# Optimization experiments

Hardware: AMD Instinct MI355X
Metric: run time of the kernel (lower is better)

## Reference

```python
import jax, jax.numpy as jnp
import numpy as np

B, L, S, M, N = 128, 3, 256, 256, 20000
NS, A, NL = 4, 5, 2
MAP_RANGE = 10.0
DELTA_VAR = 0.1
EPS = 1e-5


def _ln(x):
    mu = jnp.mean(x, -1, keepdims=True)
    var = jnp.var(x, -1, keepdims=True)
    return (x - mu) / jnp.sqrt(var + EPS)


def _cal_map_last(map_pts, anchor_last):
    # map_pts: [2, N], anchor_last: [B, 1, L] -> [B, M, 2]
    pos = anchor_last[:, 0, 0:2]
    d = map_pts[None, :, :] - pos[:, :, None]                    # [B,2,N]
    th = anchor_last[:, 0, -1]
    c, s = jnp.cos(th), jnp.sin(th)
    rot = jnp.stack([jnp.stack([c, s], -1), jnp.stack([-s, c], -1)], 1)  # [B,2,2]
    m = jnp.einsum('bij,bjn->bin', rot, d)                       # ego-frame points
    dis = jnp.sqrt(jnp.sum(m * m, axis=1, keepdims=True))        # [B,1,N]
    m = jnp.where(dis >= MAP_RANGE, 1e10, m)
    m = jnp.sort(m, axis=-1)                                     # per-coordinate sort (as in torch)
    m = jnp.where(m >= 1e9, 0.0, m)
    m = m[:, :, :M]                                              # torch F.pad negative pad == crop to map_num_max
    return jnp.transpose(m, (0, 2, 1))


def _forward(inp_start_point, map_pts, end_point, delta_limit_mean,
             W_enc_anchor, Wq, Wk, Wv, W_in, W_out, W_map1, W_map2,
             W_ih0, W_ih1, W_hh0, W_hh1, W_m1, W_m2, W_v1, W_v2):
    anchor = inp_start_point
    var_last = jnp.ones_like(anchor) * 0.01  # never updated, as in torch source
    pre_mean, pre_var, views = [], [], []
    scale = 1.0 / np.sqrt(S)                 # MHA 1 head -> head_dim = S
    bsz = anchor.shape[0]
    for step in range(NS):
        dm, dv = [anchor], [var_last]
        vt = [jnp.transpose(_cal_map_last(map_pts, anchor), (0, 2, 1))]
        h = jnp.ones((NL, bsz, S), anchor.dtype)
        c = jnp.ones((NL, bsz, S), anchor.dtype)
        for _ in range(A - 1):
            enc_a = _ln(jnp.concatenate([anchor, anchor - end_point, var_last], -1) @ W_enc_anchor[step].T)  # [B,1,S]
            ml = jax.lax.stop_gradient(_cal_map_last(map_pts, anchor))  # torch.no_grad in encode_last_map
            q = ml @ Wq[step].T
            k = ml @ Wk[step].T
            v = ml @ Wv[step].T
            wq, wk, wv = jnp.split(W_in[step], 3, axis=0)
            q2 = q @ wq.T
            k2 = k @ wk.T
            v2 = v @ wv.T
            attn = jax.nn.softmax(jnp.einsum('bqs,bks->bqk', q2, k2) * scale, axis=-1)
            o = jnp.einsum('bqk,bks->bqs', attn, v2) @ W_out[step].T    # [B,M,S]
            x = jax.nn.relu(jnp.transpose(o, (0, 2, 1)))                # [B,S,M]
            x = jax.nn.relu(x @ W_map1[step].T) @ W_map2[step].T        # [B,S,1]
            enc_m = _ln(jnp.transpose(x, (0, 2, 1)))                    # [B,1,S]
            xl = jnp.concatenate([enc_a, enc_m], -1)[:, 0, :]           # [B,2S], single LSTM timestep
            hs, cs = [], []
            for l, (Wih, Whh) in enumerate(((W_ih0[step], W_hh0[step]), (W_ih1[step], W_hh1[step]))):
                g = xl @ Wih.T + h[l] @ Whh.T
                i_g, f_g, g_g, o_g = jnp.split(g, 4, -1)               # torch gate order i,f,g,o
                cl = jax.nn.sigmoid(f_g) * c[l] + jax.nn.sigmoid(i_g) * jnp.tanh(g_g)
                hl = jax.nn.sigmoid(o_g) * jnp.tanh(cl)
                hs.append(hl)
                cs.append(cl)
                xl = hl
            h, c = jnp.stack(hs), jnp.stack(cs)
            mn = _ln(xl)[:, None, :]                                    # [B,1,S]
            mean = jnp.tanh(jax.nn.relu(jax.nn.relu(mn) @ W_m1[step].T) @ W_m2[step].T) * delta_limit_mean + anchor
            varr = jax.nn.sigmoid(jax.nn.relu(jax.nn.relu(mn) @ W_v1[step].T) @ W_v2[step].T) * DELTA_VAR
            dm.append(mean)
            dv.append(varr)
            anchor = mean
            vt.append(jnp.transpose(_cal_map_last(map_pts, anchor), (0, 2, 1)))
        pre_mean.append(jnp.concatenate(dm, 1)[:, None])    # [B,1,A,L]
        pre_var.append(jnp.concatenate(dv, 1)[:, None])
        views.append(jnp.stack(vt, 1)[:, None])             # [B,1,A,2,M]
    return (jnp.concatenate(pre_mean, 1), jnp.concatenate(pre_var, 1), jnp.concatenate(views, 1))


def setup_inputs() -> dict:
    key = jax.random.key(0)
    ks = jax.random.split(key, 20)

    def w(k, shape, fan):
        return jax.random.normal(k, shape, jnp.float32) / np.sqrt(fan)

    return {
        'inp_start_point': jax.random.normal(ks[0], (B, 1, L), jnp.float32) * 2.0,
        'map_pts': jax.random.uniform(ks[1], (2, N), jnp.float32, -50.0, 50.0),
        'end_point': jnp.array([5.0, 5.0, 0.0], jnp.float32),
        'delta_limit_mean': jnp.array([1.0, 1.0, 0.3], jnp.float32),
        'W_enc_anchor': w(ks[2], (NS, S, 3 * L), 3 * L),
        'Wq': w(ks[3], (NS, S, 2), 2),
        'Wk': w(ks[4], (NS, S, 2), 2),
        'Wv': w(ks[5], (NS, S, 2), 2),
        'W_in': w(ks[6], (NS, 3 * S, S), S),
        'W_out': w(ks[7], (NS, S, S), S),
        'W_map1': w(ks[8], (NS, S, M), M),
        'W_map2': w(ks[9], (NS, 1, S), S),
        'W_ih0': w(ks[10], (NS, 4 * S, 2 * S), 2 * S),
        'W_ih1': w(ks[11], (NS, 4 * S, S), S),
        'W_hh0': w(ks[12], (NS, 4 * S, S), S),
        'W_hh1': w(ks[13], (NS, 4 * S, S), S),
        'W_m1': w(ks[14], (NS, S, S), S),
        'W_m2': w(ks[15], (NS, L, S), S),
        'W_v1': w(ks[16], (NS, S, S), S),
        'W_v2': w(ks[17], (NS, L, S), S),
    }


def reference(inp_start_point, map_pts, end_point, delta_limit_mean,
              W_enc_anchor, Wq, Wk, Wv, W_in, W_out, W_map1, W_map2,
              W_ih0, W_ih1, W_hh0, W_hh1, W_m1, W_m2, W_v1, W_v2):
    return _forward(inp_start_point, map_pts, end_point, delta_limit_mean,
                    W_enc_anchor, Wq, Wk, Wv, W_in, W_out, W_map1, W_map2,
                    W_ih0, W_ih1, W_hh0, W_hh1, W_m1, W_m2, W_v1, W_v2)
```

## Files before the change

### kernel.cpp

```cpp
#include <hip/hip_runtime.h>

#define BB 128
#define NPTS 20000
#define NSTEP 4
#define NITER 4
#define MT 1024

#define OFF_ANCHOR 0
#define OFF_G      384
#define OFF_AO     400
#define OFF_U      2448
#define OFF_XL     67984
#define OFF_H      166288
#define OFF_C      231824
#define OFF_GB     297360
#define OFF_RMN    428432
#define OFF_TM     461200
#define OFF_TV     493968

#define OUT_VAR   7680
#define OUT_VIEWS 15360

__device__ __forceinline__ float sigf(float x){ return 1.0f/(1.0f+expf(-x)); }

__device__ __forceinline__ float blockSum256(float v, float* buf){
    for (int off = 32; off > 0; off >>= 1) v += __shfl_down(v, off, 64);
    int tid = threadIdx.x;
    __syncthreads();
    if ((tid & 63) == 0) buf[tid >> 6] = v;
    __syncthreads();
    return (buf[0] + buf[1]) + (buf[2] + buf[3]);
}

__device__ __forceinline__ float blockSum256g(float v, float* buf, int tid){
    for (int off = 32; off > 0; off >>= 1) v += __shfl_down(v, off, 64);
    __syncthreads();
    if (tid < 256 && (tid & 63) == 0) buf[tid >> 6] = v;
    __syncthreads();
    return (buf[0] + buf[1]) + (buf[2] + buf[3]);
}

__device__ __forceinline__ double blockSum256d(double v, double* buf){
    for (int off = 32; off > 0; off >>= 1) v += __shfl_down(v, off, 64);
    int tid = threadIdx.x;
    __syncthreads();
    if ((tid & 63) == 0) buf[tid >> 6] = v;
    __syncthreads();
    return (buf[0] + buf[1]) + (buf[2] + buf[3]);
}

__global__ __launch_bounds__(256) void k_init(const float* __restrict__ inp, float* __restrict__ ws)
{
    int i = blockIdx.x*256 + threadIdx.x;
    if (i < BB*3) ws[OFF_ANCHOR + i] = inp[i];
}

__global__ __launch_bounds__(256) void k_pre(const float* __restrict__ Wq, const float* __restrict__ Wk,
                                             const float* __restrict__ Wv, const float* __restrict__ Win,
                                             const float* __restrict__ Wout, float* __restrict__ ws)
{
    __shared__ float wql[512], wkl[512], wvl[512];
    __shared__ double avl[512];
    __shared__ double dbuf[4];
    int s = blockIdx.x, t = threadIdx.x;
    wql[t] = Wq[s*512 + t];   wql[256+t] = Wq[s*512 + 256 + t];
    wkl[t] = Wk[s*512 + t];   wkl[256+t] = Wk[s*512 + 256 + t];
    wvl[t] = Wv[s*512 + t];   wvl[256+t] = Wv[s*512 + 256 + t];
    __syncthreads();
    const float* wq = Win + s*196608 + t*256;
    const float* wk = wq + 65536;
    const float* wv = wq + 131072;
    double aq0=0,aq1=0,ak0=0,ak1=0,av0=0,av1=0;
    for (int j = 0; j < 256; j++){
        double a = wq[j], b = wk[j], c = wv[j];
        aq0 += a*(double)wql[j*2]; aq1 += a*(double)wql[j*2+1];
        ak0 += b*(double)wkl[j*2]; ak1 += b*(double)wkl[j*2+1];
        av0 += c*(double)wvl[j*2]; av1 += c*(double)wvl[j*2+1];
    }
    avl[t*2] = av0; avl[t*2+1] = av1;
    double g00 = blockSum256d(aq0*ak0, dbuf);
    double g01 = blockSum256d(aq0*ak1, dbuf);
    double g10 = blockSum256d(aq1*ak0, dbuf);
    double g11 = blockSum256d(aq1*ak1, dbuf);
    if (t == 0){
        ws[OFF_G + s*4+0] = (float)g00; ws[OFF_G + s*4+1] = (float)g01;
        ws[OFF_G + s*4+2] = (float)g10; ws[OFF_G + s*4+3] = (float)g11;
    }
    const float* wo = Wout + s*65536 + t*256;
    double o0 = 0.0, o1 = 0.0;
    for (int j = 0; j < 256; j++){
        double w = wo[j];
        o0 += w*avl[j*2]; o1 += w*avl[j*2+1];
    }
    ws[OFF_AO + s*512 + t*2]   = (float)o0;
    ws[OFF_AO + s*512 + t*2+1] = (float)o1;
}

__global__ __launch_bounds__(MT) void k_mapenc(const float* __restrict__ mp, float* __restrict__ ws,
                                               float* __restrict__ out, const float* __restrict__ Wenc,
                                               const float* __restrict__ endp, int s, int t, int wprev)
{
    __shared__ unsigned int histx[256], histy[256];
    __shared__ float vx[1024], vy[1024];
    __shared__ float candx[448], candy[448];
    __shared__ float mxS[256], myS[256];
    __shared__ int scanx[256], scany[256];
    __shared__ int shjx, shjy;
    __shared__ unsigned int cnt_in, cntx, cnty;
    __shared__ float rbuf[4];
    int tid = threadIdx.x, b = blockIdx.x;
    float ax = ws[OFF_ANCHOR + b*3 + 0];
    float ay = ws[OFF_ANCHOR + b*3 + 1];
    float th = ws[OFF_ANCHOR + b*3 + 2];
    float cth = cosf(th), sth = sinf(th);
    if (tid < 256){ histx[tid] = 0u; histy[tid] = 0u; }
    if (tid == 0){ cnt_in = 0u; cntx = 0u; cnty = 0u; }
    __syncthreads();
    for (int i = tid; i < NPTS; i += MT){
        float dx = mp[i] - ax, dy = mp[NPTS + i] - ay;
        float rx = cth*dx + sth*dy;
        float ry = cth*dy - sth*dx;
        float d  = sqrtf(rx*rx + ry*ry);
        if (d < 10.0f){
            unsigned p = atomicAdd(&cnt_in, 1u);
            if (p < 1024u){ vx[p] = rx; vy[p] = ry; }
            int bx = min(max((int)((rx + 10.0f)*12.8f), 0), 255);
            int by = min(max((int)((ry + 10.0f)*12.8f), 0), 255);
            atomicAdd(&histx[bx], 1u); atomicAdd(&histy[by], 1u);
        }
    }
    __syncthreads();
    int total = (int)min(cnt_in, 1024u);
    int K = min(256, total);
    int px = 0, py = 0;
    if (tid < 256){
        px = (int)histx[tid]; py = (int)histy[tid];
        scanx[tid] = px; scany[tid] = py;
    }
    __syncthreads();
    for (int off = 1; off < 256; off <<= 1){
        int vxs = 0, vys = 0;
        if (tid < 256){
            vxs = (tid >= off) ? scanx[tid - off] : 0;
            vys = (tid >= off) ? scany[tid - off] : 0;
        }
        __syncthreads();
        if (tid < 256){ scanx[tid] += vxs; scany[tid] += vys; }
        __syncthreads();
    }
    if (K > 0){
        if (tid < 256){
            if (scanx[tid] - px < K && scanx[tid] >= K) shjx = tid;
            if (scany[tid] - py < K && scany[tid] >= K) shjy = tid;
        }
    } else if (tid == 0){ shjx = -1; shjy = -1; }
    __syncthreads();
    int jx = shjx, jy = shjy;
    for (int i = tid; i < total; i += MT){
        float v = vx[i];
        int bx = min(max((int)((v + 10.0f)*12.8f), 0), 255);
        if (bx <= jx){ unsigned p = atomicAdd(&cntx, 1u); if (p < 448u) candx[p] = v; }
        v = vy[i];
        int by = min(max((int)((v + 10.0f)*12.8f), 0), 255);
        if (by <= jy){ unsigned p = atomicAdd(&cnty, 1u); if (p < 448u) candy[p] = v; }
    }
    __syncthreads();
    int cx = (int)min(cntx, 448u), cy = (int)min(cnty, 448u);
    for (int i = tid; i < cx; i += MT){
        float v = candx[i];
        int r = 0;
        for (int j2 = 0; j2 < cx; j2++){
            float w2 = candx[j2];
            r += (w2 < v) || (w2 == v && j2 < i);
        }
        if (r < 256) mxS[r] = v;
    }
    for (int i = tid; i < cy; i += MT){
        float v = candy[i];
        int r = 0;
        for (int j2 = 0; j2 < cy; j2++){
            float w2 = candy[j2];
            r += (w2 < v) || (w2 == v && j2 < i);
        }
        if (r < 256) myS[r] = v;
    }
    __syncthreads();
    float mlx = 0.f, mly = 0.f;
    if (tid < 256){
        mlx = (tid < K) ? mxS[tid] : 0.0f;
        mly = (tid < K) ? myS[tid] : 0.0f;
        int obase = OUT_VIEWS + (((b*NSTEP + s)*5 + t)*2)*256;
        out[obase + tid]       = mlx;
        out[obase + 256 + tid] = mly;
        if (wprev){
            int pbase = OUT_VIEWS + (((b*NSTEP + (s-1))*5 + 4)*2)*256;
            out[pbase + tid]       = mlx;
            out[pbase + 256 + tid] = mly;
        }
    }
    if (t == 4) return;
    __syncthreads();
    if (tid < 256){ mxS[tid] = mlx; myS[tid] = mly; }
    __syncthreads();
    float accv = 0.f, dd = 0.f;
    if (tid < 256){
        float a0 = ax, a1 = ay, a2 = th;
        float z9[9] = {a0, a1, a2, a0-endp[0], a1-endp[1], a2-endp[2], 0.01f, 0.01f, 0.01f};
        const float* w = Wenc + s*2304 + tid*9;
        #pragma unroll
        for (int j2 = 0; j2 < 9; j2++) accv += z9[j2]*w[j2];
    }
    float mu = blockSum256g(accv, rbuf, tid) * (1.0f/256.0f);
    dd = accv - mu;
    float var = blockSum256g(tid < 256 ? dd*dd : 0.f, rbuf, tid) * (1.0f/256.0f);
    if (tid < 256)
        ws[OFF_XL + b*512 + tid] = dd * rsqrtf(var + 1e-5f);
    if (tid < 256){
        float g00 = ws[OFF_G + s*4+0], g01 = ws[OFF_G + s*4+1];
        float g10 = ws[OFF_G + s*4+2], g11 = ws[OFF_G + s*4+3];
        float xq = mxS[tid], yq = myS[tid];
        float t0 = g00*xq + g10*yq;
        float t1 = g01*xq + g11*yq;
        float mxv = -1e30f;
        for (int j2 = 0; j2 < 256; j2++){
            float l = (t0*mxS[j2] + t1*myS[j2]) * 0.0625f;
            mxv = fmaxf(mxv, l);
        }
        float sum = 0.f, ux = 0.f, uy = 0.f;
        for (int j2 = 0; j2 < 256; j2++){
            float l = (t0*mxS[j2] + t1*myS[j2]) * 0.0625f;
            float e = expf(l - mxv);
            sum += e; ux += e*mxS[j2]; uy += e*myS[j2];
        }
        float inv = 1.0f/sum;
        ws[OFF_U + b*512 + tid*2]   = ux*inv;
        ws[OFF_U + b*512 + tid*2+1] = uy*inv;
        if (t == 0){
            ws[OFF_H + b*256 + tid] = 1.0f;
            ws[OFF_H + BB*256 + b*256 + tid] = 1.0f;
            ws[OFF_C + b*256 + tid] = 1.0f;
            ws[OFF_C + BB*256 + b*256 + tid] = 1.0f;
            if (tid < 3){
                out[((b*NSTEP + s)*5 + 0)*3 + tid] = ws[OFF_ANCHOR + b*3 + tid];
                out[OUT_VAR + ((b*NSTEP + s)*5 + 0)*3 + tid] = 0.01f;
            }
        }
    }
}

__global__ __launch_bounds__(256) void k_big(float* __restrict__ ws, const float* __restrict__ W1,
                                             const float* __restrict__ W2, int s)
{
    __shared__ __align__(16) float ul[512];
    __shared__ float aol[128];
    __shared__ float w2l[64];
    __shared__ __align__(16) float xt[64*36];
    __shared__ __align__(16) float w1t[64*36];
    __shared__ float red[64*17];
    int sct = blockIdx.x, st = blockIdx.y, b = blockIdx.z;
    int tid = threadIdx.x, tx = tid & 15, ty = tid >> 4;
    {
        float2 uv = *(const float2*)(ws + OFF_U + b*512 + tid*2);
        ul[tid*2] = uv.x; ul[tid*2+1] = uv.y;
        if (tid < 128) aol[tid] = ws[OFF_AO + s*512 + st*128 + tid];
        if (tid < 64)  w2l[tid] = W2[sct*64 + tid];
    }
    __syncthreads();
    float acc[4][4];
    #pragma unroll
    for (int i=0;i<4;i++){
        #pragma unroll
        for (int j=0;j<4;j++) acc[i][j] = 0.f;
    }
    for (int mt = 0; mt < 8; mt++){
        {
            int cl = tid >> 2, f0 = tid & 3;
            const float* g = W1 + (sct*64 + cl)*256 + mt*32 + f0*4;
            float4 v0 = *(const float4*)g;
            float4 v1 = *(const float4*)(g + 16);
            *(float4*)(w1t + cl*36 + f0*4)      = v0;
            *(float4*)(w1t + cl*36 + f0*4 + 16) = v1;
        }
        {
            int r = tid >> 2, mg = tid & 3;
            float A0 = aol[r*2], A1 = aol[r*2+1];
            int m0 = mt*32 + mg*4;
            float4 o0, o1;
            o0.x = fmaxf(A0*ul[(m0+0)*2] + A1*ul[(m0+0)*2+1], 0.f);
            o0.y = fmaxf(A0*ul[(m0+1)*2] + A1*ul[(m0+1)*2+1], 0.f);
            o0.z = fmaxf(A0*ul[(m0+2)*2] + A1*ul[(m0+2)*2+1], 0.f);
            o0.w = fmaxf(A0*ul[(m0+3)*2] + A1*ul[(m0+3)*2+1], 0.f);
            int m1 = mt*32 + (mg+4)*4;
            o1.x = fmaxf(A0*ul[(m1+0)*2] + A1*ul[(m1+0)*2+1], 0.f);
            o1.y = fmaxf(A0*ul[(m1+1)*2] + A1*ul[(m1+1)*2+1], 0.f);
            o1.z = fmaxf(A0*ul[(m1+2)*2] + A1*ul[(m1+2)*2+1], 0.f);
            o1.w = fmaxf(A0*ul[(m1+3)*2] + A1*ul[(m1+3)*2+1], 0.f);
            *(float4*)(xt + r*36 + mg*4)     = o0;
            *(float4*)(xt + r*36 + (mg+4)*4) = o1;
        }
        __syncthreads();
        #pragma unroll
        for (int m4 = 0; m4 < 8; m4++){
            float4 xv[4], wv[4];
            #pragma unroll
            for (int i=0;i<4;i++) xv[i] = *(const float4*)(xt + (ty + 16*i)*36 + m4*4);
            #pragma unroll
            for (int j=0;j<4;j++) wv[j] = *(const float4*)(w1t + (tx + 16*j)*36 + m4*4);
            #pragma unroll
            for (int i=0;i<4;i++){
                #pragma unroll
                for (int j=0;j<4;j++){
                    acc[i][j] += xv[i].x*wv[j].x + xv[i].y*wv[j].y + xv[i].z*wv[j].z + xv[i].w*wv[j].w;
                }
            }
        }
        __syncthreads();
    }
    #pragma unroll
    for (int i=0;i<4;i++){
        float p = 0.f;
        #pragma unroll
        for (int j=0;j<4;j++) p += fmaxf(acc[i][j], 0.f) * w2l[tx + 16*j];
        red[(ty + 16*i)*17 + tx] = p;
    }
    __syncthreads();
    if (tid < 64){
        float sm = 0.f;
        #pragma unroll
        for (int q=0;q<16;q++) sm += red[tid*17 + q];
        ws[OFF_GB + b*1024 + sct*256 + st*64 + tid] = sm;
    }
}

__global__ __launch_bounds__(256) void k_lnencm(float* __restrict__ ws)
{
    __shared__ float rbuf[4];
    int b = blockIdx.x, t = threadIdx.x;
    const float* p = ws + OFF_GB + b*1024;
    float v = p[t];
    v += p[256+t]; v += p[512+t]; v += p[768+t];
    float mu = blockSum256(v, rbuf) * (1.0f/256.0f);
    float d = v - mu;
    float var = blockSum256(d*d, rbuf) * (1.0f/256.0f);
    ws[OFF_XL + b*512 + 256 + t] = d * rsqrtf(var + 1e-5f);
}

template<int K>
__device__ __forceinline__ void gemm_pass(const float* __restrict__ A, const float* __restrict__ W,
                                          float* As, float* Wsh, float (&acc)[2][4],
                                          int bt, int ot, int tid)
{
    int tx = tid & 15, ty = tid >> 4;
    for (int kt = 0; kt < K/32; kt++){
        {
            int bb = tid >> 3, kk = (tid & 7) * 4;
            float4 v = *(const float4*)(A + (bt*32+bb)*K + kt*32 + kk);
            float* ap = As + bb*33 + kk;
            ap[0]=v.x; ap[1]=v.y; ap[2]=v.z; ap[3]=v.w;
        }
        {
            int oo = tid >> 2, kk = (tid & 3) * 8;
            const float* g = W + (ot*64+oo)*K + kt*32 + kk;
            float4 v0 = *(const float4*)g;
            float4 v1 = *(const float4*)(g + 4);
            float* wp = Wsh + oo*33 + kk;
            wp[0]=v0.x; wp[1]=v0.y; wp[2]=v0.z; wp[3]=v0.w;
            wp[4]=v1.x; wp[5]=v1.y; wp[6]=v1.z; wp[7]=v1.w;
        }
        __syncthreads();
        #pragma unroll
        for (int kk = 0; kk < 32; kk++){
            float a0 = As[(ty*2)*33 + kk], a1 = As[(ty*2+1)*33 + kk];
            float w0 = Wsh[(tx*4)*33+kk],   w1 = Wsh[(tx*4+1)*33+kk];
            float w2 = Wsh[(tx*4+2)*33+kk], w3 = Wsh[(tx*4+3)*33+kk];
            acc[0][0] += a0*w0; acc[0][1] += a0*w1; acc[0][2] += a0*w2; acc[0][3] += a0*w3;
            acc[1][0] += a1*w0; acc[1][1] += a1*w1; acc[1][2] += a1*w2; acc[1][3] += a1*w3;
        }
        __syncthreads();
    }
}

template<int K1, int K2, int RELU>
__global__ __launch_bounds__(256) void k_gemm(const float* __restrict__ A1, const float* __restrict__ W1,
                                              const float* __restrict__ A2, const float* __restrict__ W2,
                                              float* __restrict__ C, int Osz)
{
    __shared__ float As[32*33];
    __shared__ float Wsh[64*33];
    int tid = threadIdx.x, tx = tid & 15, ty = tid >> 4;
    int ot = blockIdx.x, bt = blockIdx.y;
    float acc[2][4];
    #pragma unroll
    for (int i=0;i<2;i++){
        #pragma unroll
        for (int j=0;j<4;j++) acc[i][j]=0.f;
    }
    gemm_pass<K1>(A1, W1, As, Wsh, acc, bt, ot, tid);
    if constexpr (K2 > 0){
        gemm_pass<K2>(A2, W2, As, Wsh, acc, bt, ot, tid);
    }
    #pragma unroll
    for (int i=0;i<2;i++){
        float4 v;
        v.x = acc[i][0]; v.y = acc[i][1]; v.z = acc[i][2]; v.w = acc[i][3];
        if (RELU){ v.x=fmaxf(v.x,0.f); v.y=fmaxf(v.y,0.f); v.z=fmaxf(v.z,0.f); v.w=fmaxf(v.w,0.f); }
        *(float4*)(C + (bt*32+ty*2+i)*Osz + ot*64 + tx*4) = v;
    }
}

__global__ __launch_bounds__(256) void k_heads2(const float* __restrict__ A, const float* __restrict__ Wm1,
                                                const float* __restrict__ Wv1, float* __restrict__ ws)
{
    __shared__ float As[32*33];
    __shared__ float Wsh[64*33];
    int tid = threadIdx.x, tx = tid & 15, ty = tid >> 4;
    int bx = blockIdx.x, bt = blockIdx.y;
    int ot = bx & 3;
    const float* W = (bx < 4) ? Wm1 : Wv1;
    float* C = ws + ((bx < 4) ? OFF_TM : OFF_TV);
    float acc[2][4];
    #pragma unroll
    for (int i=0;i<2;i++){
        #pragma unroll
        for (int j=0;j<4;j++) acc[i][j]=0.f;
    }
    gemm_pass<256>(A, W, As, Wsh, acc, bt, ot, tid);
    #pragma unroll
    for (int i=0;i<2;i++){
        float4 v;
        v.x = fmaxf(acc[i][0],0.f); v.y = fmaxf(acc[i][1],0.f);
        v.z = fmaxf(acc[i][2],0.f); v.w = fmaxf(acc[i][3],0.f);
        *(float4*)(C + (bt*32+ty*2+i)*256 + ot*64 + tx*4) = v;
    }
}

__global__ __launch_bounds__(256) void k_gates(float* __restrict__ ws, int l)
{
    int b = blockIdx.x, t = threadIdx.x;
    const float* g = ws + OFF_GB + b*1024;
    float ig = g[t], fg = g[256+t], gg = g[512+t], og = g[768+t];
    int idx = l*BB*256 + b*256 + t;
    float cold = ws[OFF_C + idx];
    float cl = sigf(fg)*cold + sigf(ig)*tanhf(gg);
    float hl = sigf(og)*tanhf(cl);
    ws[OFF_C + idx] = cl;
    ws[OFF_H + idx] = hl;
}

__global__ __launch_bounds__(256) void k_mn(float* __restrict__ ws)
{
    __shared__ float rbuf[4];
    int b = blockIdx.x, t = threadIdx.x;
    const float* g = ws + OFF_GB + b*1024;
    float ig = g[t], fg = g[256+t], gg = g[512+t], og = g[768+t];
    int idx = BB*256 + b*256 + t;
    float cold = ws[OFF_C + idx];
    float cl = sigf(fg)*cold + sigf(ig)*tanhf(gg);
    float hl = sigf(og)*tanhf(cl);
    ws[OFF_C + idx] = cl;
    ws[OFF_H + idx] = hl;
    float mu = blockSum256(hl, rbuf) * (1.0f/256.0f);
    float d = hl - mu;
    float var = blockSum256(d*d, rbuf) * (1.0f/256.0f);
    ws[OFF_RMN + b*256 + t] = fmaxf(d * rsqrtf(var + 1e-5f), 0.0f);
}

__global__ __launch_bounds__(256) void k_head(const float* __restrict__ Wm2, const float* __restrict__ Wv2,
                                              const float* __restrict__ dlm, float* __restrict__ ws,
                                              float* __restrict__ out, int s, int t)
{
    int b = blockIdx.x, tid = threadIdx.x;
    int w = tid >> 6, lane = tid & 63;
    #pragma unroll
    for (int p = 0; p < 2; p++){
        int oi = p*4 + w;
        if (oi < 6){
            int j = (oi < 3) ? oi : oi - 3;
            const float* tb = ws + ((oi < 3) ? OFF_TM : OFF_TV) + b*256;
            const float* wr = ((oi < 3) ? Wm2 : Wv2) + j*256;
            float pa = 0.f;
            #pragma unroll
            for (int q = 0; q < 4; q++) pa += tb[lane + 64*q] * wr[lane + 64*q];
            for (int off = 32; off > 0; off >>= 1) pa += __shfl_down(pa, off, 64);
            if (lane == 0){
                if (oi < 3){
                    float mv = tanhf(pa) * dlm[j] + ws[OFF_ANCHOR + b*3 + j];
                    out[((b*NSTEP + s)*5 + (t+1))*3 + j] = mv;
                    ws[OFF_ANCHOR + b*3 + j] = mv;
                } else {
                    out[OUT_VAR + ((b*NSTEP + s)*5 + (t+1))*3 + j] = sigf(pa)*0.1f;
                }
            }
        }
    }
}

extern "C" void kernel_launch(void* const* d_in, const int* in_sizes, int n_in,
                              void* d_out, int out_size, void* d_ws, size_t ws_size,
                              hipStream_t stream)
{
    (void)in_sizes; (void)n_in; (void)out_size; (void)ws_size;
    const float* inp  = (const float*)d_in[0];
    const float* mp   = (const float*)d_in[1];
    const float* endp = (const float*)d_in[2];
    const float* dlm  = (const float*)d_in[3];
    const float* Wenc = (const float*)d_in[4];
    const float* Wq   = (const float*)d_in[5];
    const float* Wk   = (const float*)d_in[6];
    const float* Wv   = (const float*)d_in[7];
    const float* Win  = (const float*)d_in[8];
    const float* Wout = (const float*)d_in[9];
    const float* Wmap1= (const float*)d_in[10];
    const float* Wmap2= (const float*)d_in[11];
    const float* Wih0 = (const float*)d_in[12];
    const float* Wih1 = (const float*)d_in[13];
    const float* Whh0 = (const float*)d_in[14];
    const float* Whh1 = (const float*)d_in[15];
    const float* Wm1  = (const float*)d_in[16];
    const float* Wm2  = (const float*)d_in[17];
    const float* Wv1  = (const float*)d_in[18];
    const float* Wv2  = (const float*)d_in[19];
    float* out = (float*)d_out;
    float* ws  = (float*)d_ws;

    k_init<<<2, 256, 0, stream>>>(inp, ws);
    k_pre<<<NSTEP, 256, 0, stream>>>(Wq, Wk, Wv, Win, Wout, ws);
    for (int s = 0; s < NSTEP; s++){
        for (int t = 0; t < NITER; t++){
            k_mapenc<<<BB, MT, 0, stream>>>(mp, ws, out, Wenc, endp, s, t,
                                            (t == 0 && s > 0) ? 1 : 0);
            k_big<<<dim3(4, 4, BB), 256, 0, stream>>>(ws, Wmap1 + s*65536, Wmap2 + s*256, s);
            k_lnencm<<<BB, 256, 0, stream>>>(ws);
            k_gemm<512,256,0><<<dim3(16,4), 256, 0, stream>>>(ws+OFF_XL, Wih0 + s*524288,
                                                              ws+OFF_H,  Whh0 + s*262144,
                                                              ws+OFF_GB, 1024);
            k_gates<<<BB, 256, 0, stream>>>(ws, 0);
            k_gemm<256,256,0><<<dim3(16,4), 256, 0, stream>>>(ws+OFF_H,          Wih1 + s*262144,
                                                              ws+OFF_H + BB*256, Whh1 + s*262144,
                                                              ws+OFF_GB, 1024);
            k_mn<<<BB, 256, 0, stream>>>(ws);
            k_heads2<<<dim3(8,4), 256, 0, stream>>>(ws+OFF_RMN, Wm1 + s*65536, Wv1 + s*65536, ws);
            k_head<<<BB, 256, 0, stream>>>(Wm2 + s*768, Wv2 + s*768, dlm, ws, out, s, t);
        }
    }
    k_mapenc<<<BB, MT, 0, stream>>>(mp, ws, out, Wenc, endp, 3, 4, 0);
}
```

Before: 3.742 ms.

## Fuse LSTM, gate and head tail kernels into one cooperative kernel with grid syncs

Replaces the seven small per-iteration tail kernels (layer norm, two LSTM GEMMs, gates, norm, head GEMMs, final head) with a single cooperative kernel of 64 blocks that uses grid-wide syncs between phases. The aim is to cut kernel launch overhead and inter-kernel gaps across the 16 iterations. In exchange, the elementwise phases now run on 64 blocks, each handling two batch rows, where they previously had 128. Each grid.sync also has its own cost.

```diff
diff --git a/kernel.cpp b/kernel.cpp
--- a/kernel.cpp
+++ b/kernel.cpp
@@ -1,4 +1,7 @@
 #include <hip/hip_runtime.h>
+#include <hip/hip_cooperative_groups.h>
+
+namespace cg = cooperative_groups;
 
 #define BB 128
 #define NPTS 20000
@@ -332,19 +335,6 @@
     }
 }
 
-__global__ __launch_bounds__(256) void k_lnencm(float* __restrict__ ws)
-{
-    __shared__ float rbuf[4];
-    int b = blockIdx.x, t = threadIdx.x;
-    const float* p = ws + OFF_GB + b*1024;
-    float v = p[t];
-    v += p[256+t]; v += p[512+t]; v += p[768+t];
-    float mu = blockSum256(v, rbuf) * (1.0f/256.0f);
-    float d = v - mu;
-    float var = blockSum256(d*d, rbuf) * (1.0f/256.0f);
-    ws[OFF_XL + b*512 + 256 + t] = d * rsqrtf(var + 1e-5f);
-}
-
 template<int K>
 __device__ __forceinline__ void gemm_pass(const float* __restrict__ A, const float* __restrict__ W,
                                           float* As, float* Wsh, float (&acc)[2][4],
@@ -380,115 +370,145 @@
     }
 }
 
-template<int K1, int K2, int RELU>
-__global__ __launch_bounds__(256) void k_gemm(const float* __restrict__ A1, const float* __restrict__ W1,
-                                              const float* __restrict__ A2, const float* __restrict__ W2,
-                                              float* __restrict__ C, int Osz)
-{
+__global__ __launch_bounds__(256) void k_tail(
+    const float* __restrict__ Wih0, const float* __restrict__ Whh0,
+    const float* __restrict__ Wih1, const float* __restrict__ Whh1,
+    const float* __restrict__ Wm1, const float* __restrict__ Wv1,
+    const float* __restrict__ Wm2, const float* __restrict__ Wv2,
+    const float* __restrict__ dlm, float* __restrict__ ws, float* __restrict__ out,
+    int s, int t)
+{
+    cg::grid_group grid = cg::this_grid();
     __shared__ float As[32*33];
     __shared__ float Wsh[64*33];
-    int tid = threadIdx.x, tx = tid & 15, ty = tid >> 4;
-    int ot = blockIdx.x, bt = blockIdx.y;
-    float acc[2][4];
-    #pragma unroll
-    for (int i=0;i<2;i++){
-        #pragma unroll
-        for (int j=0;j<4;j++) acc[i][j]=0.f;
-    }
-    gemm_pass<K1>(A1, W1, As, Wsh, acc, bt, ot, tid);
-    if constexpr (K2 > 0){
-        gemm_pass<K2>(A2, W2, As, Wsh, acc, bt, ot, tid);
-    }
-    #pragma unroll
-    for (int i=0;i<2;i++){
-        float4 v;
-        v.x = acc[i][0]; v.y = acc[i][1]; v.z = acc[i][2]; v.w = acc[i][3];
-        if (RELU){ v.x=fmaxf(v.x,0.f); v.y=fmaxf(v.y,0.f); v.z=fmaxf(v.z,0.f); v.w=fmaxf(v.w,0.f); }
-        *(float4*)(C + (bt*32+ty*2+i)*Osz + ot*64 + tx*4) = v;
-    }
-}
-
-__global__ __launch_bounds__(256) void k_heads2(const float* __restrict__ A, const float* __restrict__ Wm1,
-                                                const float* __restrict__ Wv1, float* __restrict__ ws)
-{
-    __shared__ float As[32*33];
-    __shared__ float Wsh[64*33];
-    int tid = threadIdx.x, tx = tid & 15, ty = tid >> 4;
-    int bx = blockIdx.x, bt = blockIdx.y;
-    int ot = bx & 3;
-    const float* W = (bx < 4) ? Wm1 : Wv1;
-    float* C = ws + ((bx < 4) ? OFF_TM : OFF_TV);
-    float acc[2][4];
-    #pragma unroll
-    for (int i=0;i<2;i++){
-        #pragma unroll
-        for (int j=0;j<4;j++) acc[i][j]=0.f;
-    }
-    gemm_pass<256>(A, W, As, Wsh, acc, bt, ot, tid);
-    #pragma unroll
-    for (int i=0;i<2;i++){
-        float4 v;
-        v.x = fmaxf(acc[i][0],0.f); v.y = fmaxf(acc[i][1],0.f);
-        v.z = fmaxf(acc[i][2],0.f); v.w = fmaxf(acc[i][3],0.f);
-        *(float4*)(C + (bt*32+ty*2+i)*256 + ot*64 + tx*4) = v;
-    }
-}
-
-__global__ __launch_bounds__(256) void k_gates(float* __restrict__ ws, int l)
-{
-    int b = blockIdx.x, t = threadIdx.x;
-    const float* g = ws + OFF_GB + b*1024;
-    float ig = g[t], fg = g[256+t], gg = g[512+t], og = g[768+t];
-    int idx = l*BB*256 + b*256 + t;
-    float cold = ws[OFF_C + idx];
-    float cl = sigf(fg)*cold + sigf(ig)*tanhf(gg);
-    float hl = sigf(og)*tanhf(cl);
-    ws[OFF_C + idx] = cl;
-    ws[OFF_H + idx] = hl;
-}
-
-__global__ __launch_bounds__(256) void k_mn(float* __restrict__ ws)
-{
     __shared__ float rbuf[4];
-    int b = blockIdx.x, t = threadIdx.x;
-    const float* g = ws + OFF_GB + b*1024;
-    float ig = g[t], fg = g[256+t], gg = g[512+t], og = g[768+t];
-    int idx = BB*256 + b*256 + t;
-    float cold = ws[OFF_C + idx];
-    float cl = sigf(fg)*cold + sigf(ig)*tanhf(gg);
-    float hl = sigf(og)*tanhf(cl);
-    ws[OFF_C + idx] = cl;
-    ws[OFF_H + idx] = hl;
-    float mu = blockSum256(hl, rbuf) * (1.0f/256.0f);
-    float d = hl - mu;
-    float var = blockSum256(d*d, rbuf) * (1.0f/256.0f);
-    ws[OFF_RMN + b*256 + t] = fmaxf(d * rsqrtf(var + 1e-5f), 0.0f);
-}
-
-__global__ __launch_bounds__(256) void k_head(const float* __restrict__ Wm2, const float* __restrict__ Wv2,
-                                              const float* __restrict__ dlm, float* __restrict__ ws,
-                                              float* __restrict__ out, int s, int t)
-{
-    int b = blockIdx.x, tid = threadIdx.x;
-    int w = tid >> 6, lane = tid & 63;
-    #pragma unroll
-    for (int p = 0; p < 2; p++){
-        int oi = p*4 + w;
-        if (oi < 6){
-            int j = (oi < 3) ? oi : oi - 3;
-            const float* tb = ws + ((oi < 3) ? OFF_TM : OFF_TV) + b*256;
-            const float* wr = ((oi < 3) ? Wm2 : Wv2) + j*256;
-            float pa = 0.f;
+    int g = blockIdx.x, tid = threadIdx.x;
+    int tx = tid & 15, ty = tid >> 4;
+
+    for (int bb = 0; bb < 2; bb++){
+        int b = g*2 + bb;
+        const float* p = ws + OFF_GB + b*1024;
+        float v = p[tid];
+        v += p[256+tid]; v += p[512+tid]; v += p[768+tid];
+        float mu = blockSum256(v, rbuf) * (1.0f/256.0f);
+        float d = v - mu;
+        float var = blockSum256(d*d, rbuf) * (1.0f/256.0f);
+        ws[OFF_XL + b*512 + 256 + tid] = d * rsqrtf(var + 1e-5f);
+    }
+    grid.sync();
+
+    {
+        int ot = g & 15, bt = g >> 4;
+        float acc[2][4];
+        #pragma unroll
+        for (int i=0;i<2;i++){
             #pragma unroll
-            for (int q = 0; q < 4; q++) pa += tb[lane + 64*q] * wr[lane + 64*q];
-            for (int off = 32; off > 0; off >>= 1) pa += __shfl_down(pa, off, 64);
-            if (lane == 0){
-                if (oi < 3){
-                    float mv = tanhf(pa) * dlm[j] + ws[OFF_ANCHOR + b*3 + j];
-                    out[((b*NSTEP + s)*5 + (t+1))*3 + j] = mv;
-                    ws[OFF_ANCHOR + b*3 + j] = mv;
-                } else {
-                    out[OUT_VAR + ((b*NSTEP + s)*5 + (t+1))*3 + j] = sigf(pa)*0.1f;
+            for (int j=0;j<4;j++) acc[i][j]=0.f;
+        }
+        gemm_pass<512>(ws + OFF_XL, Wih0, As, Wsh, acc, bt, ot, tid);
+        gemm_pass<256>(ws + OFF_H,  Whh0, As, Wsh, acc, bt, ot, tid);
+        #pragma unroll
+        for (int i=0;i<2;i++){
+            float4 v;
+            v.x = acc[i][0]; v.y = acc[i][1]; v.z = acc[i][2]; v.w = acc[i][3];
+            *(float4*)(ws + OFF_GB + (bt*32+ty*2+i)*1024 + ot*64 + tx*4) = v;
+        }
+    }
+    grid.sync();
+
+    for (int bb = 0; bb < 2; bb++){
+        int b = g*2 + bb;
+        const float* gg_ = ws + OFF_GB + b*1024;
+        float ig = gg_[tid], fg = gg_[256+tid], ggv = gg_[512+tid], og = gg_[768+tid];
+        int idx = b*256 + tid;
+        float cold = ws[OFF_C + idx];
+        float cl = sigf(fg)*cold + sigf(ig)*tanhf(ggv);
+        float hl = sigf(og)*tanhf(cl);
+        ws[OFF_C + idx] = cl;
+        ws[OFF_H + idx] = hl;
+    }
+    grid.sync();
+
+    {
+        int ot = g & 15, bt = g >> 4;
+        float acc[2][4];
+        #pragma unroll
+        for (int i=0;i<2;i++){
+            #pragma unroll
+            for (int j=0;j<4;j++) acc[i][j]=0.f;
+        }
+        gemm_pass<256>(ws + OFF_H,          Wih1, As, Wsh, acc, bt, ot, tid);
+        gemm_pass<256>(ws + OFF_H + BB*256, Whh1, As, Wsh, acc, bt, ot, tid);
+        #pragma unroll
+        for (int i=0;i<2;i++){
+            float4 v;
+            v.x = acc[i][0]; v.y = acc[i][1]; v.z = acc[i][2]; v.w = acc[i][3];
+            *(float4*)(ws + OFF_GB + (bt*32+ty*2+i)*1024 + ot*64 + tx*4) = v;
+        }
+    }
+    grid.sync();
+
+    for (int bb = 0; bb < 2; bb++){
+        int b = g*2 + bb;
+        const float* gg_ = ws + OFF_GB + b*1024;
+        float ig = gg_[tid], fg = gg_[256+tid], ggv = gg_[512+tid], og = gg_[768+tid];
+        int idx = BB*256 + b*256 + tid;
+        float cold = ws[OFF_C + idx];
+        float cl = sigf(fg)*cold + sigf(ig)*tanhf(ggv);
+        float hl = sigf(og)*tanhf(cl);
+        ws[OFF_C + idx] = cl;
+        ws[OFF_H + idx] = hl;
+        float mu = blockSum256(hl, rbuf) * (1.0f/256.0f);
+        float d = hl - mu;
+        float var = blockSum256(d*d, rbuf) * (1.0f/256.0f);
+        ws[OFF_RMN + b*256 + tid] = fmaxf(d * rsqrtf(var + 1e-5f), 0.0f);
+    }
+    grid.sync();
+
+    if (g < 32){
+        int bx = g & 7, bt = g >> 3;
+        int ot = bx & 3;
+        const float* W = (bx < 4) ? Wm1 : Wv1;
+        float* C = ws + ((bx < 4) ? OFF_TM : OFF_TV);
+        float acc[2][4];
+        #pragma unroll
+        for (int i=0;i<2;i++){
+            #pragma unroll
+            for (int j=0;j<4;j++) acc[i][j]=0.f;
+        }
+        gemm_pass<256>(ws + OFF_RMN, W, As, Wsh, acc, bt, ot, tid);
+        #pragma unroll
+        for (int i=0;i<2;i++){
+            float4 v;
+            v.x = fmaxf(acc[i][0],0.f); v.y = fmaxf(acc[i][1],0.f);
+            v.z = fmaxf(acc[i][2],0.f); v.w = fmaxf(acc[i][3],0.f);
+            *(float4*)(C + (bt*32+ty*2+i)*256 + ot*64 + tx*4) = v;
+        }
+    }
+    grid.sync();
+
+    for (int bb = 0; bb < 2; bb++){
+        int b = g*2 + bb;
+        int w = tid >> 6, lane = tid & 63;
+        #pragma unroll
+        for (int p = 0; p < 2; p++){
+            int oi = p*4 + w;
+            if (oi < 6){
+                int j = (oi < 3) ? oi : oi - 3;
+                const float* tb = ws + ((oi < 3) ? OFF_TM : OFF_TV) + b*256;
+                const float* wr = ((oi < 3) ? Wm2 : Wv2) + j*256;
+                float pa = 0.f;
+                #pragma unroll
+                for (int q = 0; q < 4; q++) pa += tb[lane + 64*q] * wr[lane + 64*q];
+                for (int off = 32; off > 0; off >>= 1) pa += __shfl_down(pa, off, 64);
+                if (lane == 0){
+                    if (oi < 3){
+                        float mv = tanhf(pa) * dlm[j] + ws[OFF_ANCHOR + b*3 + j];
+                        out[((b*NSTEP + s)*5 + (t+1))*3 + j] = mv;
+                        ws[OFF_ANCHOR + b*3 + j] = mv;
+                    } else {
+                        out[OUT_VAR + ((b*NSTEP + s)*5 + (t+1))*3 + j] = sigf(pa)*0.1f;
+                    }
                 }
             }
         }
@@ -530,17 +550,25 @@
             k_mapenc<<<BB, MT, 0, stream>>>(mp, ws, out, Wenc, endp, s, t,
                                             (t == 0 && s > 0) ? 1 : 0);
             k_big<<<dim3(4, 4, BB), 256, 0, stream>>>(ws, Wmap1 + s*65536, Wmap2 + s*256, s);
-            k_lnencm<<<BB, 256, 0, stream>>>(ws);
-            k_gemm<512,256,0><<<dim3(16,4), 256, 0, stream>>>(ws+OFF_XL, Wih0 + s*524288,
-                                                              ws+OFF_H,  Whh0 + s*262144,
-                                                              ws+OFF_GB, 1024);
-            k_gates<<<BB, 256, 0, stream>>>(ws, 0);
-            k_gemm<256,256,0><<<dim3(16,4), 256, 0, stream>>>(ws+OFF_H,          Wih1 + s*262144,
-                                                              ws+OFF_H + BB*256, Whh1 + s*262144,
-                                                              ws+OFF_GB, 1024);
-            k_mn<<<BB, 256, 0, stream>>>(ws);
-            k_heads2<<<dim3(8,4), 256, 0, stream>>>(ws+OFF_RMN, Wm1 + s*65536, Wv1 + s*65536, ws);
-            k_head<<<BB, 256, 0, stream>>>(Wm2 + s*768, Wv2 + s*768, dlm, ws, out, s, t);
+            {
+                const float* a_ih0 = Wih0 + s*524288;
+                const float* a_hh0 = Whh0 + s*262144;
+                const float* a_ih1 = Wih1 + s*262144;
+                const float* a_hh1 = Whh1 + s*262144;
+                const float* a_m1  = Wm1 + s*65536;
+                const float* a_v1  = Wv1 + s*65536;
+                const float* a_m2  = Wm2 + s*768;
+                const float* a_v2  = Wv2 + s*768;
+                const float* a_dlm = dlm;
+                float* a_ws = ws;
+                float* a_out = out;
+                int sv = s, tv = t;
+                void* args[13] = {(void*)&a_ih0, (void*)&a_hh0, (void*)&a_ih1, (void*)&a_hh1,
+                                  (void*)&a_m1, (void*)&a_v1, (void*)&a_m2, (void*)&a_v2,
+                                  (void*)&a_dlm, (void*)&a_ws, (void*)&a_out, (void*)&sv, (void*)&tv};
+                hipLaunchCooperativeKernel((const void*)k_tail, dim3(64), dim3(256),
+                                           args, 0, stream);
+            }
         }
     }
     k_mapenc<<<BB, MT, 0, stream>>>(mp, ws, out, Wenc, endp, 3, 4, 0);
```

New measurement: 4.883 ms. +30.5%, slower.

## Fuse LSTM gates into layer-1 GEMM and merge heads; aggregate atomics per wavefront

Applied to the files above, without the earlier changes.

The layer-0 gate nonlinearity is folded into the layer-1 GEMM kernel. Each block recomputes h0 for its 32 batch rows into shared memory, and the cell state is ping-ponged between two buffers so blocks with different output tiles do not race on it. The layer-1 gates, layernorm, both head GEMMs and the final projections are fused into one per-batch kernel. This cuts five launches per iteration to two. In the map encoder, per-thread shared atomics are replaced with ballot and popcount wavefront-aggregated atomics. The cost is that gate math is now computed redundantly 16 times, and the per-batch kernel streams the full Wm1/Wv1 matrices once per batch row instead of sharing tiles across rows.

```diff
diff --git a/kernel.cpp b/kernel.cpp
--- a/kernel.cpp
+++ b/kernel.cpp
@@ -14,9 +14,8 @@
 #define OFF_H      166288
 #define OFF_C      231824
 #define OFF_GB     297360
-#define OFF_RMN    428432
-#define OFF_TM     461200
-#define OFF_TV     493968
+#define OFF_C0B    428432
+#define OFF_GB2    461200
 
 #define OUT_VAR   7680
 #define OUT_VIEWS 15360
@@ -109,6 +108,7 @@
     __shared__ unsigned int cnt_in, cntx, cnty;
     __shared__ float rbuf[4];
     int tid = threadIdx.x, b = blockIdx.x;
+    int lane = tid & 63;
     float ax = ws[OFF_ANCHOR + b*3 + 0];
     float ay = ws[OFF_ANCHOR + b*3 + 1];
     float th = ws[OFF_ANCHOR + b*3 + 2];
@@ -121,8 +121,15 @@
         float rx = cth*dx + sth*dy;
         float ry = cth*dy - sth*dx;
         float d  = sqrtf(rx*rx + ry*ry);
-        if (d < 10.0f){
-            unsigned p = atomicAdd(&cnt_in, 1u);
+        bool keep = (d < 10.0f);
+        unsigned long long mask = __ballot(keep);
+        if (keep){
+            unsigned long long lower = mask & ((1ull << lane) - 1ull);
+            int leader = __ffsll((unsigned long long)mask) - 1;
+            unsigned base = 0;
+            if (lane == leader) base = atomicAdd(&cnt_in, (unsigned)__popcll(mask));
+            base = __shfl(base, leader, 64);
+            unsigned p = base + (unsigned)__popcll(lower);
             if (p < 1024u){ vx[p] = rx; vy[p] = ry; }
             int bx = min(max((int)((rx + 10.0f)*12.8f), 0), 255);
             int by = min(max((int)((ry + 10.0f)*12.8f), 0), 255);
@@ -157,12 +164,30 @@
     __syncthreads();
     int jx = shjx, jy = shjy;
     for (int i = tid; i < total; i += MT){
-        float v = vx[i];
-        int bx = min(max((int)((v + 10.0f)*12.8f), 0), 255);
-        if (bx <= jx){ unsigned p = atomicAdd(&cntx, 1u); if (p < 448u) candx[p] = v; }
-        v = vy[i];
-        int by = min(max((int)((v + 10.0f)*12.8f), 0), 255);
-        if (by <= jy){ unsigned p = atomicAdd(&cnty, 1u); if (p < 448u) candy[p] = v; }
+        float vxa = vx[i], vya = vy[i];
+        int bx = min(max((int)((vxa + 10.0f)*12.8f), 0), 255);
+        int by = min(max((int)((vya + 10.0f)*12.8f), 0), 255);
+        bool kx = (bx <= jx), ky = (by <= jy);
+        unsigned long long mx_ = __ballot(kx);
+        if (kx){
+            unsigned long long lower = mx_ & ((1ull << lane) - 1ull);
+            int leader = __ffsll((unsigned long long)mx_) - 1;
+            unsigned base = 0;
+            if (lane == leader) base = atomicAdd(&cntx, (unsigned)__popcll(mx_));
+            base = __shfl(base, leader, 64);
+            unsigned p = base + (unsigned)__popcll(lower);
+            if (p < 448u) candx[p] = vxa;
+        }
+        unsigned long long my_ = __ballot(ky);
+        if (ky){
+            unsigned long long lower = my_ & ((1ull << lane) - 1ull);
+            int leader = __ffsll((unsigned long long)my_) - 1;
+            unsigned base = 0;
+            if (lane == leader) base = atomicAdd(&cnty, (unsigned)__popcll(my_));
+            base = __shfl(base, leader, 64);
+            unsigned p = base + (unsigned)__popcll(lower);
+            if (p < 448u) candy[p] = vya;
+        }
     }
     __syncthreads();
     int cx = (int)min(cntx, 448u), cy = (int)min(cnty, 448u);
@@ -380,6 +405,18 @@
     }
 }
 
+template<int K>
+__device__ __forceinline__ void stage_w(const float* __restrict__ W, float* Wsh, int ot, int kt, int tid)
+{
+    int oo = tid >> 2, kk = (tid & 3) * 8;
+    const float* g = W + (ot*64+oo)*K + kt*32 + kk;
+    float4 v0 = *(const float4*)g;
+    float4 v1 = *(const float4*)(g + 4);
+    float* wp = Wsh + oo*33 + kk;
+    wp[0]=v0.x; wp[1]=v0.y; wp[2]=v0.z; wp[3]=v0.w;
+    wp[4]=v1.x; wp[5]=v1.y; wp[6]=v1.z; wp[7]=v1.w;
+}
+
 template<int K1, int K2, int RELU>
 __global__ __launch_bounds__(256) void k_gemm(const float* __restrict__ A1, const float* __restrict__ W1,
                                               const float* __restrict__ A2, const float* __restrict__ W2,
@@ -408,87 +445,130 @@
     }
 }
 
-__global__ __launch_bounds__(256) void k_heads2(const float* __restrict__ A, const float* __restrict__ Wm1,
-                                                const float* __restrict__ Wv1, float* __restrict__ ws)
-{
+__global__ __launch_bounds__(256) void k_g256(const float* __restrict__ Wih1, const float* __restrict__ Whh1,
+                                              float* __restrict__ ws, int t)
+{
+    __shared__ float h0t[32*257];
     __shared__ float As[32*33];
     __shared__ float Wsh[64*33];
     int tid = threadIdx.x, tx = tid & 15, ty = tid >> 4;
-    int bx = blockIdx.x, bt = blockIdx.y;
-    int ot = bx & 3;
-    const float* W = (bx < 4) ? Wm1 : Wv1;
-    float* C = ws + ((bx < 4) ? OFF_TM : OFF_TV);
+    int ot = blockIdx.x, bt = blockIdx.y;
+    int crd = (t & 1) ? OFF_C0B : OFF_C;
+    int cwr = (t & 1) ? OFF_C : OFF_C0B;
+    for (int bb = 0; bb < 32; bb++){
+        int b = bt*32 + bb;
+        const float* g = ws + OFF_GB + b*1024;
+        float ig = g[tid], fg = g[256+tid], gg = g[512+tid], og = g[768+tid];
+        float cold = ws[crd + b*256 + tid];
+        float cl = sigf(fg)*cold + sigf(ig)*tanhf(gg);
+        float hl = sigf(og)*tanhf(cl);
+        ws[cwr + b*256 + tid] = cl;
+        ws[OFF_H + b*256 + tid] = hl;
+        h0t[bb*257 + tid] = hl;
+    }
+    __syncthreads();
     float acc[2][4];
     #pragma unroll
     for (int i=0;i<2;i++){
         #pragma unroll
         for (int j=0;j<4;j++) acc[i][j]=0.f;
     }
-    gemm_pass<256>(A, W, As, Wsh, acc, bt, ot, tid);
+    for (int kt = 0; kt < 8; kt++){
+        stage_w<256>(Wih1, Wsh, ot, kt, tid);
+        __syncthreads();
+        #pragma unroll
+        for (int kk = 0; kk < 32; kk++){
+            float a0 = h0t[(ty*2)*257 + kt*32 + kk], a1 = h0t[(ty*2+1)*257 + kt*32 + kk];
+            float w0 = Wsh[(tx*4)*33+kk],   w1 = Wsh[(tx*4+1)*33+kk];
+            float w2 = Wsh[(tx*4+2)*33+kk], w3 = Wsh[(tx*4+3)*33+kk];
+            acc[0][0] += a0*w0; acc[0][1] += a0*w1; acc[0][2] += a0*w2; acc[0][3] += a0*w3;
+            acc[1][0] += a1*w0; acc[1][1] += a1*w1; acc[1][2] += a1*w2; acc[1][3] += a1*w3;
+        }
+        __syncthreads();
+    }
+    gemm_pass<256>(ws + OFF_H + BB*256, Whh1, As, Wsh, acc, bt, ot, tid);
     #pragma unroll
     for (int i=0;i<2;i++){
         float4 v;
-        v.x = fmaxf(acc[i][0],0.f); v.y = fmaxf(acc[i][1],0.f);
-        v.z = fmaxf(acc[i][2],0.f); v.w = fmaxf(acc[i][3],0.f);
-        *(float4*)(C + (bt*32+ty*2+i)*256 + ot*64 + tx*4) = v;
-    }
-}
-
-__global__ __launch_bounds__(256) void k_gates(float* __restrict__ ws, int l)
-{
-    int b = blockIdx.x, t = threadIdx.x;
-    const float* g = ws + OFF_GB + b*1024;
-    float ig = g[t], fg = g[256+t], gg = g[512+t], og = g[768+t];
-    int idx = l*BB*256 + b*256 + t;
-    float cold = ws[OFF_C + idx];
-    float cl = sigf(fg)*cold + sigf(ig)*tanhf(gg);
-    float hl = sigf(og)*tanhf(cl);
-    ws[OFF_C + idx] = cl;
-    ws[OFF_H + idx] = hl;
-}
-
-__global__ __launch_bounds__(256) void k_mn(float* __restrict__ ws)
-{
+        v.x = acc[i][0]; v.y = acc[i][1]; v.z = acc[i][2]; v.w = acc[i][3];
+        *(float4*)(ws + OFF_GB2 + (bt*32+ty*2+i)*1024 + ot*64 + tx*4) = v;
+    }
+}
+
+__global__ __launch_bounds__(256) void k_tailb(const float* __restrict__ Wm1, const float* __restrict__ Wv1,
+                                               const float* __restrict__ Wm2, const float* __restrict__ Wv2,
+                                               const float* __restrict__ dlm, float* __restrict__ ws,
+                                               float* __restrict__ out, int s, int t)
+{
+    __shared__ float rmn[256];
+    __shared__ float tml[256], tvl[256];
+    __shared__ float Wsh2[256*33];
     __shared__ float rbuf[4];
-    int b = blockIdx.x, t = threadIdx.x;
-    const float* g = ws + OFF_GB + b*1024;
-    float ig = g[t], fg = g[256+t], gg = g[512+t], og = g[768+t];
-    int idx = BB*256 + b*256 + t;
-    float cold = ws[OFF_C + idx];
-    float cl = sigf(fg)*cold + sigf(ig)*tanhf(gg);
-    float hl = sigf(og)*tanhf(cl);
-    ws[OFF_C + idx] = cl;
-    ws[OFF_H + idx] = hl;
-    float mu = blockSum256(hl, rbuf) * (1.0f/256.0f);
-    float d = hl - mu;
-    float var = blockSum256(d*d, rbuf) * (1.0f/256.0f);
-    ws[OFF_RMN + b*256 + t] = fmaxf(d * rsqrtf(var + 1e-5f), 0.0f);
-}
-
-__global__ __launch_bounds__(256) void k_head(const float* __restrict__ Wm2, const float* __restrict__ Wv2,
-                                              const float* __restrict__ dlm, float* __restrict__ ws,
-                                              float* __restrict__ out, int s, int t)
-{
     int b = blockIdx.x, tid = threadIdx.x;
-    int w = tid >> 6, lane = tid & 63;
-    #pragma unroll
-    for (int p = 0; p < 2; p++){
-        int oi = p*4 + w;
-        if (oi < 6){
-            int j = (oi < 3) ? oi : oi - 3;
-            const float* tb = ws + ((oi < 3) ? OFF_TM : OFF_TV) + b*256;
-            const float* wr = ((oi < 3) ? Wm2 : Wv2) + j*256;
-            float pa = 0.f;
+    {
+        const float* g = ws + OFF_GB2 + b*1024;
+        float ig = g[tid], fg = g[256+tid], gg = g[512+tid], og = g[768+tid];
+        int idx = BB*256 + b*256 + tid;
+        float cold = ws[OFF_C + idx];
+        float cl = sigf(fg)*cold + sigf(ig)*tanhf(gg);
+        float hl = sigf(og)*tanhf(cl);
+        ws[OFF_C + idx] = cl;
+        ws[OFF_H + idx] = hl;
+        float mu = blockSum256(hl, rbuf) * (1.0f/256.0f);
+        float d = hl - mu;
+        float var = blockSum256(d*d, rbuf) * (1.0f/256.0f);
+        rmn[tid] = fmaxf(d * rsqrtf(var + 1e-5f), 0.0f);
+    }
+    __syncthreads();
+    float am = 0.f, av = 0.f;
+    for (int pass = 0; pass < 2; pass++){
+        const float* W = pass ? Wv1 : Wm1;
+        float a = 0.f;
+        for (int kt = 0; kt < 8; kt++){
+            {
+                int o = (tid >> 3);
+                int kk = (tid & 7)*4;
+                #pragma unroll
+                for (int r8 = 0; r8 < 8; r8++){
+                    int oo = r8*32 + o;
+                    float4 v = *(const float4*)(W + oo*256 + kt*32 + kk);
+                    float* wp = Wsh2 + oo*33 + kk;
+                    wp[0]=v.x; wp[1]=v.y; wp[2]=v.z; wp[3]=v.w;
+                }
+            }
+            __syncthreads();
             #pragma unroll
-            for (int q = 0; q < 4; q++) pa += tb[lane + 64*q] * wr[lane + 64*q];
-            for (int off = 32; off > 0; off >>= 1) pa += __shfl_down(pa, off, 64);
-            if (lane == 0){
-                if (oi < 3){
-                    float mv = tanhf(pa) * dlm[j] + ws[OFF_ANCHOR + b*3 + j];
-                    out[((b*NSTEP + s)*5 + (t+1))*3 + j] = mv;
-                    ws[OFF_ANCHOR + b*3 + j] = mv;
-                } else {
-                    out[OUT_VAR + ((b*NSTEP + s)*5 + (t+1))*3 + j] = sigf(pa)*0.1f;
+            for (int kk = 0; kk < 32; kk++){
+                a += rmn[kt*32 + kk] * Wsh2[tid*33 + kk];
+            }
+            __syncthreads();
+        }
+        if (pass == 0) am = a; else av = a;
+    }
+    tml[tid] = fmaxf(am, 0.f);
+    tvl[tid] = fmaxf(av, 0.f);
+    __syncthreads();
+    {
+        int w = tid >> 6, lane = tid & 63;
+        #pragma unroll
+        for (int p = 0; p < 2; p++){
+            int oi = p*4 + w;
+            if (oi < 6){
+                int j = (oi < 3) ? oi : oi - 3;
+                const float* tb = (oi < 3) ? tml : tvl;
+                const float* wr = ((oi < 3) ? Wm2 : Wv2) + j*256;
+                float pa = 0.f;
+                #pragma unroll
+                for (int q = 0; q < 4; q++) pa += tb[lane + 64*q] * wr[lane + 64*q];
+                for (int off = 32; off > 0; off >>= 1) pa += __shfl_down(pa, off, 64);
+                if (lane == 0){
+                    if (oi < 3){
+                        float mv = tanhf(pa) * dlm[j] + ws[OFF_ANCHOR + b*3 + j];
+                        out[((b*NSTEP + s)*5 + (t+1))*3 + j] = mv;
+                        ws[OFF_ANCHOR + b*3 + j] = mv;
+                    } else {
+                        out[OUT_VAR + ((b*NSTEP + s)*5 + (t+1))*3 + j] = sigf(pa)*0.1f;
+                    }
                 }
             }
         }
@@ -534,13 +614,9 @@
             k_gemm<512,256,0><<<dim3(16,4), 256, 0, stream>>>(ws+OFF_XL, Wih0 + s*524288,
                                                               ws+OFF_H,  Whh0 + s*262144,
                                                               ws+OFF_GB, 1024);
-            k_gates<<<BB, 256, 0, stream>>>(ws, 0);
-            k_gemm<256,256,0><<<dim3(16,4), 256, 0, stream>>>(ws+OFF_H,          Wih1 + s*262144,
-                                                              ws+OFF_H + BB*256, Whh1 + s*262144,
-                                                              ws+OFF_GB, 1024);
-            k_mn<<<BB, 256, 0, stream>>>(ws);
-            k_heads2<<<dim3(8,4), 256, 0, stream>>>(ws+OFF_RMN, Wm1 + s*65536, Wv1 + s*65536, ws);
-            k_head<<<BB, 256, 0, stream>>>(Wm2 + s*768, Wv2 + s*768, dlm, ws, out, s, t);
+            k_g256<<<dim3(16,4), 256, 0, stream>>>(Wih1 + s*262144, Whh1 + s*262144, ws, t);
+            k_tailb<<<BB, 256, 0, stream>>>(Wm1 + s*65536, Wv1 + s*65536,
+                                            Wm2 + s*768, Wv2 + s*768, dlm, ws, out, s, t);
         }
     }
     k_mapenc<<<BB, MT, 0, stream>>>(mp, ws, out, Wenc, endp, 3, 4, 0);
```

New measurement: 4.037 ms. 1.08x slower.
